# Kernel optimization log

Hardware: AMD Instinct MI355X
Metric: run time of the kernel (lower is better)

## Reference

```python
import jax, jax.numpy as jnp
import numpy as np

D_MODEL = 512
KERNEL = 16
DILATIONS = (1, 1, 2, 2, 4, 4, 8, 8)
HEADS = len(DILATIONS)
HEAD_W = D_MODEL // HEADS
B, L = 2, 1024
MODE = "forward"  # causal: window sees only prior words


def setup_inputs() -> dict:
    key = jax.random.key(0)
    ks = jax.random.split(key, 8)
    s = 0.02  # small init like nn.Linear
    return {
        "tensor": jax.random.normal(ks[0], (B, L, D_MODEL), jnp.float32),
        "Wq": jax.random.normal(ks[1], (HEADS, HEAD_W, D_MODEL), jnp.float32) * s,
        "bq": jnp.zeros((HEADS, HEAD_W), jnp.float32),
        "Wk": jax.random.normal(ks[2], (HEADS, KERNEL, HEAD_W, D_MODEL), jnp.float32) * s,
        "bk": jnp.zeros((HEADS, KERNEL, HEAD_W), jnp.float32),
        "Wv": jax.random.normal(ks[3], (HEADS, KERNEL, HEAD_W, D_MODEL), jnp.float32) * s,
        "bv": jnp.zeros((HEADS, KERNEL, HEAD_W), jnp.float32),
        "Wo": jax.random.normal(ks[4], (D_MODEL, HEADS, HEAD_W), jnp.float32) * s,
        "bo": jnp.zeros((D_MODEL,), jnp.float32),
    }


def _window_indices():
    """Static gather indices replicating Glimpses.dilocal's dilated unfold.

    Returns idx of shape (H, L, K) indexing into a sequence zero-padded by
    max_off on both sides: content[h, l, k] = x_padded[idx[h, l, k]].
    """
    dil = np.asarray(DILATIONS)  # (H,)
    max_off = int((KERNEL - 1) * dil.max())
    if MODE == "forward":
        front = (KERNEL - 1) * dil           # all padding in front (causal)
    elif MODE == "backward":
        front = np.zeros_like(dil)           # all padding behind
    else:  # center
        front = ((KERNEL - 1) * dil) // 2
    l = np.arange(L)[None, :, None]
    k = np.arange(KERNEL)[None, None, :]
    d = dil[:, None, None]
    f = front[:, None, None]
    idx = l + k * d - f + max_off            # (H, L, K), always in-range
    return jnp.asarray(idx), max_off


_IDX, _MOFF = _window_indices()


def reference(tensor, Wq, bq, Wk, bk, Wv, bv, Wo, bo):
    # tensor: (B, L, D)
    xp = jnp.pad(tensor, ((0, 0), (_MOFF, _MOFF), (0, 0)))
    content = xp[:, _IDX, :]                                   # (B,H,L,K,D)
    # per-head query projection (kernel position 1)
    q = jnp.einsum('bld,hod->bhlo', tensor, Wq) + bq[:, None, :]        # (B,H,L,hw)
    # per-(head, kernel-position) independent key/value projections
    k = jnp.einsum('bhlkd,hkod->bhlko', content, Wk) + bk[:, None, :, :]
    v = jnp.einsum('bhlkd,hkod->bhlko', content, Wv) + bv[:, None, :, :]
    # tiny local attention over the K window positions
    logits = jnp.einsum('bhlo,bhlko->bhlk', q, k)               # (B,H,L,K)
    score = jax.nn.softmax(logits, axis=-1)
    # NOTE: original scales AFTER the score@value matmul (faithful to source)
    attn = jnp.einsum('bhlk,bhlko->bhlo', score, v)
    attn = attn / jnp.sqrt(jnp.asarray(HEAD_W, tensor.dtype))   # (B,H,L,hw)
    # dehead: merge (heads, head_width) -> d_model
    out = jnp.einsum('bhlo,dho->bld', attn, Wo) + bo            # (B,L,D)
    return out
```

## Files before the change

### kernel.cpp

```cpp
#include <hip/hip_runtime.h>


#define BD 2
#define LL 1024
#define DM 512
#define HH 8
#define KT 16
#define HW 64

#define NQKV 16896

typedef unsigned short u16;
typedef unsigned int u32;
typedef __bf16 bf16x8 __attribute__((ext_vector_type(8)));
typedef float f32x4 __attribute__((ext_vector_type(4)));
typedef unsigned short ushort4v __attribute__((ext_vector_type(4)));
typedef unsigned short ushort8v __attribute__((ext_vector_type(8)));

__constant__ int c_dil[8] = {1, 1, 2, 2, 4, 4, 8, 8};

__device__ __forceinline__ float bf2f(u16 u) {
    return __builtin_bit_cast(float, (u32)u << 16);
}
__device__ __forceinline__ u16 f2bf(float f) {
    u32 u = __builtin_bit_cast(u32, f);
    return (u16)((u + 0x7fffu + ((u >> 16) & 1u)) >> 16);
}

__device__ __forceinline__ void gl_lds16(const u16* g, u16* l) {
    __builtin_amdgcn_global_load_lds(
        (__attribute__((address_space(1))) void*)g,
        (__attribute__((address_space(3))) void*)l, 16, 0, 0);
}

__global__ __launch_bounds__(256, 4) void gemm_bf16(
    const u16* __restrict__ A, const u16* __restrict__ Bm,
    const float* __restrict__ bq, const float* __restrict__ bk,
    const float* __restrict__ bv, u16* __restrict__ C)
{
    const int bid = blockIdx.x;
    const int wg  = (bid & 7) * 264 + (bid >> 3);
    const int m0  = (wg & 15) << 7;
    const int n0  = (wg >> 4) << 7;

    __shared__ u16 As[2][128 * 32];
    __shared__ u16 Bs[2][128 * 32];

    const int tid  = threadIdx.x;
    const int wave = tid >> 6, lane = tid & 63;
    const int r0 = tid >> 2;
    const int cc = (tid & 3) << 3;
    const int mw = (wave >> 1) << 6;
    const int nw = (wave & 1) << 6;
    const int lr = lane & 15;
    const int qg = lane >> 4;
    const int ksw = ((qg ^ ((lr >> 1) & 3)) << 3);

    const u16* Ag = A  + (size_t)(m0 + r0) * DM + cc;
    const u16* Bg = Bm + (size_t)(n0 + r0) * DM + cc;
    u16* lA = &As[0][0] + tid * 8;
    u16* lB = &Bs[0][0] + tid * 8;

#define STG(ko, c) do {                                                    \
        gl_lds16(Ag + (ko),                  lA + (c) * 4096);             \
        gl_lds16(Ag + (ko) + (size_t)64*DM,  lA + (c) * 4096 + 2048);      \
        gl_lds16(Bg + (ko),                  lB + (c) * 4096);             \
        gl_lds16(Bg + (ko) + (size_t)64*DM,  lB + (c) * 4096 + 2048);      \
    } while (0)

    f32x4 acc[4][4];
#pragma unroll
    for (int i = 0; i < 4; ++i)
#pragma unroll
        for (int j = 0; j < 4; ++j) acc[i][j] = (f32x4){0.f, 0.f, 0.f, 0.f};

    STG(0, 0);
    __syncthreads();

#pragma unroll
    for (int kc = 0; kc < 16; ++kc) {
        const int cur = kc & 1;
        if (kc < 15) STG((kc + 1) << 5, cur ^ 1);

        bf16x8 af[4], bfr[4];
#pragma unroll
        for (int i = 0; i < 4; ++i)
            af[i] = *(const bf16x8*)&As[cur][(mw + (i << 4) + lr) * 32 + ksw];
#pragma unroll
        for (int j = 0; j < 4; ++j)
            bfr[j] = *(const bf16x8*)&Bs[cur][(nw + (j << 4) + lr) * 32 + ksw];
#pragma unroll
        for (int i = 0; i < 4; ++i)
#pragma unroll
            for (int j = 0; j < 4; ++j)
                acc[i][j] = __builtin_amdgcn_mfma_f32_16x16x32_bf16(
                    af[i], bfr[j], acc[i][j], 0, 0, 0);

        __syncthreads();
    }
#undef STG

    const float* bias; int cb;
    if      (n0 <  512) { bias = bq; cb = 0;    }
    else if (n0 < 8704) { bias = bk; cb = 512;  }
    else                { bias = bv; cb = 8704; }

#pragma unroll
    for (int i = 0; i < 4; ++i) {
        const int rowb = m0 + mw + (i << 4) + (qg << 2);
#pragma unroll
        for (int j = 0; j < 4; ++j) {
            const int col = n0 + nw + (j << 4) + lr;
            const float bs = bias[col - cb];
#pragma unroll
            for (int r = 0; r < 4; ++r)
                C[(size_t)(rowb + r) * NQKV + col] = f2bf(acc[i][j][r] + bs);
        }
    }
}

__global__ __launch_bounds__(256, 4) void gemm_out(
    const u16* __restrict__ A, const u16* __restrict__ Bm,
    const float* __restrict__ bias, float* __restrict__ C)
{
    __shared__ u16 As[2][64 * 32];
    __shared__ u16 Bs[2][64 * 32];

    const int tid  = threadIdx.x;
    const int wave = tid >> 6, lane = tid & 63;
    const int m0 = blockIdx.y << 6, n0 = blockIdx.x << 6;
    const int r0 = tid >> 2, cc = (tid & 3) << 3;
    const int mw = wave << 4;
    const int lr = lane & 15, qg = lane >> 4;
    const int ksw = ((qg ^ ((lr >> 1) & 3)) << 3);

    const u16* Ag = A  + (size_t)(m0 + r0) * DM + cc;
    const u16* Bg = Bm + (size_t)(n0 + r0) * DM + cc;
    u16* lA = &As[0][0] + tid * 8;
    u16* lB = &Bs[0][0] + tid * 8;

#define STG(ko, c) do {                                                    \
        gl_lds16(Ag + (ko), lA + (c) * 2048);                              \
        gl_lds16(Bg + (ko), lB + (c) * 2048);                              \
    } while (0)

    f32x4 acc[4];
#pragma unroll
    for (int j = 0; j < 4; ++j) acc[j] = (f32x4){0.f, 0.f, 0.f, 0.f};

    STG(0, 0);
    __syncthreads();

#pragma unroll
    for (int kc = 0; kc < 16; ++kc) {
        const int cur = kc & 1;
        if (kc < 15) STG((kc + 1) << 5, cur ^ 1);

        bf16x8 af = *(const bf16x8*)&As[cur][(mw + lr) * 32 + ksw];
#pragma unroll
        for (int j = 0; j < 4; ++j) {
            bf16x8 bfr = *(const bf16x8*)&Bs[cur][((j << 4) + lr) * 32 + ksw];
            acc[j] = __builtin_amdgcn_mfma_f32_16x16x32_bf16(af, bfr, acc[j], 0, 0, 0);
        }
        __syncthreads();
    }
#undef STG

#pragma unroll
    for (int j = 0; j < 4; ++j) {
        const int col = n0 + (j << 4) + lr;
        const float bs = bias[col];
#pragma unroll
        for (int r = 0; r < 4; ++r)
            C[(size_t)(m0 + mw + (qg << 2) + r) * DM + col] = acc[j][r] + bs;
    }
}

__global__ void cvt_swz(const float* __restrict__ x,  const float* __restrict__ Wq,
                        const float* __restrict__ Wk, const float* __restrict__ Wv,
                        const float* __restrict__ Wo,
                        u16* __restrict__ xb, u16* __restrict__ wb,
                        u16* __restrict__ wob)
{
    const int i = blockIdx.x * 256 + threadIdx.x;
    const float* src; u16* dst; int t;
    if (i < 131072) {
        t = i;
        src = x;  dst = xb;
    } else if (i < 1212416) {
        t = i - 131072;
        const int row = t >> 6;
        if      (row <  512) src = Wq;
        else if (row < 8704) src = Wk - (size_t)512 * DM;
        else                 src = Wv - (size_t)8704 * DM;
        dst = wb;
    } else {
        t = i - 1212416;
        src = Wo; dst = wob;
    }
    const int row = t >> 6;
    const int c8  = t & 63;
    const int s   = (row >> 1) & 3;
    const int oc  = (c8 & ~3) | ((c8 & 3) ^ s);
    const float* p = src + (size_t)row * DM + (oc << 3);
    float4 v0 = *(const float4*)p;
    float4 v1 = *(const float4*)(p + 4);
    ushort8v o = { f2bf(v0.x), f2bf(v0.y), f2bf(v0.z), f2bf(v0.w),
                   f2bf(v1.x), f2bf(v1.y), f2bf(v1.z), f2bf(v1.w) };
    *(ushort8v*)(dst + (size_t)row * DM + (c8 << 3)) = o;
}

__global__ __launch_bounds__(256, 4) void attn_bf16(
    const u16* __restrict__ qkv,
    const float* __restrict__ bk,
    const float* __restrict__ bv,
    u16* __restrict__ attnb)
{
    const int tid = threadIdx.x;
    const int j  = tid & 7;
    const int ll = tid >> 3;
    const int bid = blockIdx.x;
    const int h = bid & 7;
    const int t = (bid >> 3) & 31;
    const int b = bid >> 8;
    const int l = (t << 5) + ll;
    const int dil = c_dil[h];

    const int hko = h * (KT * HW);
    const size_t rowbase = (size_t)(b * LL) * NQKV + hko + (j << 3);

    float qf[8];
    {
        ushort8v qv = *(const ushort8v*)(qkv + (size_t)(b * LL + l) * NQKV
                                         + h * HW + (j << 3));
#pragma unroll
        for (int z = 0; z < 8; ++z) qf[z] = bf2f(qv[z]);
    }

    ushort8v kr[KT];
#pragma unroll
    for (int k = 0; k < KT; ++k) {
        const int src = l - (KT - 1 - k) * dil;
        if (src >= 0)
            kr[k] = *(const ushort8v*)(qkv + rowbase + (size_t)src * NQKV
                                       + 512 + k * HW);
    }

    float lg[KT];
#pragma unroll
    for (int k = 0; k < KT; ++k) {
        const int src = l - (KT - 1 - k) * dil;
        float p = 0.f;
        if (src >= 0) {
#pragma unroll
            for (int z = 0; z < 8; ++z) p += qf[z] * bf2f(kr[k][z]);
        } else {
            const float* bkp = bk + hko + k * HW + (j << 3);
#pragma unroll
            for (int z = 0; z < 8; ++z) p += qf[z] * bkp[z];
        }
        p += __shfl_xor(p, 1);
        p += __shfl_xor(p, 2);
        p += __shfl_xor(p, 4);
        lg[k] = p;
    }

    float m = lg[0];
#pragma unroll
    for (int k = 1; k < KT; ++k) m = fmaxf(m, lg[k]);
    float s = 0.f;
#pragma unroll
    for (int k = 0; k < KT; ++k) { lg[k] = __expf(lg[k] - m); s += lg[k]; }
    const float inv = 1.f / s;

    ushort8v vr[KT];
#pragma unroll
    for (int k = 0; k < KT; ++k) {
        const int src = l - (KT - 1 - k) * dil;
        if (src >= 0)
            vr[k] = *(const ushort8v*)(qkv + rowbase + (size_t)src * NQKV
                                       + 8704 + k * HW);
    }

    float acc[8];
#pragma unroll
    for (int z = 0; z < 8; ++z) acc[z] = 0.f;
#pragma unroll
    for (int k = 0; k < KT; ++k) {
        const int src = l - (KT - 1 - k) * dil;
        const float sc = lg[k] * inv;
        if (src >= 0) {
#pragma unroll
            for (int z = 0; z < 8; ++z) acc[z] = fmaf(sc, bf2f(vr[k][z]), acc[z]);
        } else {
            const float* bvp = bv + hko + k * HW + (j << 3);
#pragma unroll
            for (int z = 0; z < 8; ++z) acc[z] = fmaf(sc, bvp[z], acc[z]);
        }
    }

    ushort8v o;
#pragma unroll
    for (int z = 0; z < 8; ++z) o[z] = f2bf(acc[z] * 0.125f);
    const int row = b * LL + l;
    const int k8 = h * 8 + j;
    const int sw = ((k8 & 3) ^ ((l >> 1) & 3)) << 3;
    *(ushort8v*)(attnb + (size_t)row * DM + ((k8 >> 2) << 5) + sw) = o;
}

__global__ __launch_bounds__(256, 2) void gemm_nt_bias(
    const float* __restrict__ A, const float* __restrict__ Bm,
    const float* __restrict__ bias, float* __restrict__ C,
    int M, int N, int Kd)
{
    __shared__ float As[16][68];
    __shared__ float Bs[16][68];
    const int tid = threadIdx.x;
    const int tx = tid & 15, ty = tid >> 4;
    const int r0 = blockIdx.y << 6, c0 = blockIdx.x << 6;
    const int lr = tid >> 2, k4 = (tid & 3) << 2;
    const float* Ap = A  + (size_t)(r0 + lr) * Kd + k4;
    const float* Bp = Bm + (size_t)(c0 + lr) * Kd + k4;
    float acc[4][4];
#pragma unroll
    for (int i = 0; i < 4; ++i)
#pragma unroll
        for (int j = 0; j < 4; ++j) acc[i][j] = 0.f;
    for (int d0 = 0; d0 < Kd; d0 += 16) {
        float4 av = *(const float4*)(Ap + d0);
        float4 bv = *(const float4*)(Bp + d0);
        As[k4 + 0][lr] = av.x; As[k4 + 1][lr] = av.y;
        As[k4 + 2][lr] = av.z; As[k4 + 3][lr] = av.w;
        Bs[k4 + 0][lr] = bv.x; Bs[k4 + 1][lr] = bv.y;
        Bs[k4 + 2][lr] = bv.z; Bs[k4 + 3][lr] = bv.w;
        __syncthreads();
#pragma unroll
        for (int dd = 0; dd < 16; ++dd) {
            float4 a4 = *(const float4*)&As[dd][ty << 2];
            float4 b4 = *(const float4*)&Bs[dd][tx << 2];
            float ar[4] = {a4.x, a4.y, a4.z, a4.w};
            float br[4] = {b4.x, b4.y, b4.z, b4.w};
#pragma unroll
            for (int i = 0; i < 4; ++i)
#pragma unroll
                for (int j = 0; j < 4; ++j)
                    acc[i][j] = fmaf(ar[i], br[j], acc[i][j]);
        }
        __syncthreads();
    }
#pragma unroll
    for (int i = 0; i < 4; ++i) {
        float4 o;
        const int c = c0 + (tx << 2);
        o.x = acc[i][0] + bias[c + 0];
        o.y = acc[i][1] + bias[c + 1];
        o.z = acc[i][2] + bias[c + 2];
        o.w = acc[i][3] + bias[c + 3];
        *(float4*)&C[(size_t)(r0 + (ty << 2) + i) * N + c] = o;
    }
}

__device__ __forceinline__ void tile_gemm_f32(
    const float* __restrict__ xb, int src, bool ok,
    const float* __restrict__ wrow,
    int lr, int k4, int tx, int ty,
    float (&As)[16][68], float (&Ws)[16][68], float (&acc)[4][4])
{
#pragma unroll
    for (int i = 0; i < 4; ++i)
#pragma unroll
        for (int j = 0; j < 4; ++j) acc[i][j] = 0.f;
    const float* xrow = xb + (size_t)(ok ? src : 0) * DM + k4;
    for (int d0 = 0; d0 < DM; d0 += 16) {
        float4 av = make_float4(0.f, 0.f, 0.f, 0.f);
        if (ok) av = *(const float4*)(xrow + d0);
        float4 wv = *(const float4*)(wrow + d0);
        As[k4 + 0][lr] = av.x; As[k4 + 1][lr] = av.y;
        As[k4 + 2][lr] = av.z; As[k4 + 3][lr] = av.w;
        Ws[k4 + 0][lr] = wv.x; Ws[k4 + 1][lr] = wv.y;
        Ws[k4 + 2][lr] = wv.z; Ws[k4 + 3][lr] = wv.w;
        __syncthreads();
#pragma unroll
        for (int dd = 0; dd < 16; ++dd) {
            float4 a4 = *(const float4*)&As[dd][ty << 2];
            float4 b4 = *(const float4*)&Ws[dd][tx << 2];
            float ar[4] = {a4.x, a4.y, a4.z, a4.w};
            float br[4] = {b4.x, b4.y, b4.z, b4.w};
#pragma unroll
            for (int i = 0; i < 4; ++i)
#pragma unroll
                for (int j = 0; j < 4; ++j)
                    acc[i][j] = fmaf(ar[i], br[j], acc[i][j]);
        }
        __syncthreads();
    }
}

__global__ __launch_bounds__(256, 2) void attn_kernel(
    const float* __restrict__ x, const float* __restrict__ q,
    const float* __restrict__ Wk, const float* __restrict__ bk,
    const float* __restrict__ Wv, const float* __restrict__ bv,
    float* __restrict__ attn)
{
    __shared__ float As[16][68];
    __shared__ float Ws[16][68];
    __shared__ float qs[64][68];
    __shared__ float lg[64][17];
    __shared__ float red[64][17];
    const int tid = threadIdx.x;
    const int tx = tid & 15, ty = tid >> 4;
    const int bid = blockIdx.x;
    const int h = bid & 7, t = (bid >> 3) & 15, b = bid >> 7;
    const int l0 = t << 6;
    const int dil = c_dil[h];
    const int lr = tid >> 2, k4 = (tid & 3) << 2;
    for (int i = tid; i < 64 * 16; i += 256) {
        int l = i >> 4, o4 = (i & 15) << 2;
        float4 v = *(const float4*)&q[((size_t)(b * LL + l0 + l) * HH + h) * HW + o4];
        *(float4*)&qs[l][o4] = v;
    }
    const float* xb  = x  + (size_t)b * LL * DM;
    const float* Wkh = Wk + (size_t)h * KT * HW * DM;
    const float* Wvh = Wv + (size_t)h * KT * HW * DM;
    const float* bkh = bk + h * KT * HW;
    const float* bvh = bv + h * KT * HW;
    float acc[4][4];
    for (int kk = 0; kk < KT; ++kk) {
        const int src = l0 + lr - (KT - 1 - kk) * dil;
        const bool ok = (src >= 0) && (src < LL);
        tile_gemm_f32(xb, src, ok, Wkh + (size_t)(kk * HW + lr) * DM + k4,
                      lr, k4, tx, ty, As, Ws, acc);
        const float* bkp = bkh + kk * HW + (tx << 2);
#pragma unroll
        for (int i = 0; i < 4; ++i) {
            float p = 0.f;
#pragma unroll
            for (int j = 0; j < 4; ++j)
                p += (acc[i][j] + bkp[j]) * qs[(ty << 2) + i][(tx << 2) + j];
            red[(ty << 2) + i][tx] = p;
        }
        __syncthreads();
        if (tid < 64) {
            float s = 0.f;
#pragma unroll
            for (int u = 0; u < 16; ++u) s += red[tid][u];
            lg[tid][kk] = s;
        }
        __syncthreads();
    }
    if (tid < 64) {
        float m = lg[tid][0];
#pragma unroll
        for (int u = 1; u < KT; ++u) m = fmaxf(m, lg[tid][u]);
        float s = 0.f;
#pragma unroll
        for (int u = 0; u < KT; ++u) {
            float e = expf(lg[tid][u] - m);
            lg[tid][u] = e; s += e;
        }
        float inv = 1.f / s;
#pragma unroll
        for (int u = 0; u < KT; ++u) lg[tid][u] *= inv;
    }
    __syncthreads();
    float vacc[4][4];
#pragma unroll
    for (int i = 0; i < 4; ++i)
#pragma unroll
        for (int j = 0; j < 4; ++j) vacc[i][j] = 0.f;
    for (int kk = 0; kk < KT; ++kk) {
        const int src = l0 + lr - (KT - 1 - kk) * dil;
        const bool ok = (src >= 0) && (src < LL);
        tile_gemm_f32(xb, src, ok, Wvh + (size_t)(kk * HW + lr) * DM + k4,
                      lr, k4, tx, ty, As, Ws, acc);
        const float* bvp = bvh + kk * HW + (tx << 2);
#pragma unroll
        for (int i = 0; i < 4; ++i) {
            float sc = lg[(ty << 2) + i][kk];
#pragma unroll
            for (int j = 0; j < 4; ++j)
                vacc[i][j] = fmaf(sc, acc[i][j] + bvp[j], vacc[i][j]);
        }
    }
#pragma unroll
    for (int i = 0; i < 4; ++i) {
        float4 o;
        o.x = vacc[i][0] * 0.125f;
        o.y = vacc[i][1] * 0.125f;
        o.z = vacc[i][2] * 0.125f;
        o.w = vacc[i][3] * 0.125f;
        *(float4*)&attn[((size_t)(b * LL + l0 + (ty << 2) + i) * HH + h) * HW + (tx << 2)] = o;
    }
}

extern "C" void kernel_launch(void* const* d_in, const int* in_sizes, int n_in,
                              void* d_out, int out_size, void* d_ws, size_t ws_size,
                              hipStream_t stream)
{
    const float* x  = (const float*)d_in[0];
    const float* Wq = (const float*)d_in[1];
    const float* bq = (const float*)d_in[2];
    const float* Wk = (const float*)d_in[3];
    const float* bk = (const float*)d_in[4];
    const float* Wv = (const float*)d_in[5];
    const float* bv = (const float*)d_in[6];
    const float* Wo = (const float*)d_in[7];
    const float* bo = (const float*)d_in[8];
    float* out = (float*)d_out;

    const int M = BD * LL;

    const size_t N_X   = (size_t)BD * LL * DM;
    const size_t N_WB  = (size_t)NQKV * DM;
    const size_t N_WO  = (size_t)DM * DM;
    const size_t N_QKV = (size_t)M * NQKV;
    const size_t NEED  = (N_X + N_WB + N_WO + N_QKV + N_X) * 2;

    if (ws_size >= NEED) {
        u16* xb    = (u16*)d_ws;
        u16* wb    = xb    + N_X;
        u16* wob   = wb    + N_WB;
        u16* qkv   = wob   + N_WO;
        u16* attnb = qkv   + N_QKV;

        cvt_swz<<<4864, 256, 0, stream>>>(x, Wq, Wk, Wv, Wo, xb, wb, wob);

        gemm_bf16<<<dim3(2112), 256, 0, stream>>>(
            xb, wb, bq, bk, bv, qkv);

        attn_bf16<<<BD * HH * (LL / 32), 256, 0, stream>>>(
            qkv, bk, bv, attnb);

        gemm_out<<<dim3(8, 32), 256, 0, stream>>>(attnb, wob, bo, out);
    } else {
        float* qws = (float*)d_ws;
        float* aws = qws + (size_t)BD * LL * HH * HW;
        gemm_nt_bias<<<dim3((HH * HW) / 64, M / 64), 256, 0, stream>>>(
            x, Wq, bq, qws, M, HH * HW, DM);
        attn_kernel<<<BD * HH * (LL / 64), 256, 0, stream>>>(
            x, qws, Wk, bk, Wv, bv, aws);
        gemm_nt_bias<<<dim3(DM / 64, M / 64), 256, 0, stream>>>(
            aws, Wo, bo, out, M, DM, HH * HW);
    }
}
```

Before: 171.5 us.

## Store K/V projections in per-slot contiguous layout for attention gathers

The QKV GEMM epilogue now writes Q into its own [M,512] buffer and scatters K and V into a [kv][head][kslot][batch][L][64] layout instead of one row-major [M,16896] matrix. In the attention kernel, each window gather then reads 64-element contiguous rows inside a compact per-(head,slot) plane, rather than striding by 16896 elements per row. This should improve cache and TLB locality for the dilated gathers. In exchange, the GEMM stores are scattered across planes with per-row index arithmetic, which may coalesce less well.

```diff
diff --git a/kernel.cpp b/kernel.cpp
--- a/kernel.cpp
+++ b/kernel.cpp
@@ -36,7 +36,8 @@
 __global__ __launch_bounds__(256, 4) void gemm_bf16(
     const u16* __restrict__ A, const u16* __restrict__ Bm,
     const float* __restrict__ bq, const float* __restrict__ bk,
-    const float* __restrict__ bv, u16* __restrict__ C)
+    const float* __restrict__ bv,
+    u16* __restrict__ qb, u16* __restrict__ kvb)
 {
     const int bid = blockIdx.x;
     const int wg  = (bid & 7) * 264 + (bid >> 3);
@@ -100,21 +101,43 @@
     }
 #undef STG
 
-    const float* bias; int cb;
-    if      (n0 <  512) { bias = bq; cb = 0;    }
-    else if (n0 < 8704) { bias = bk; cb = 512;  }
-    else                { bias = bv; cb = 8704; }
-
-#pragma unroll
-    for (int i = 0; i < 4; ++i) {
-        const int rowb = m0 + mw + (i << 4) + (qg << 2);
-#pragma unroll
-        for (int j = 0; j < 4; ++j) {
-            const int col = n0 + nw + (j << 4) + lr;
-            const float bs = bias[col - cb];
-#pragma unroll
-            for (int r = 0; r < 4; ++r)
-                C[(size_t)(rowb + r) * NQKV + col] = f2bf(acc[i][j][r] + bs);
+    if (n0 < 512) {
+#pragma unroll
+        for (int i = 0; i < 4; ++i) {
+            const int rowb = m0 + mw + (i << 4) + (qg << 2);
+#pragma unroll
+            for (int j = 0; j < 4; ++j) {
+                const int col = n0 + nw + (j << 4) + lr;
+                const float bs = bq[col];
+#pragma unroll
+                for (int r = 0; r < 4; ++r)
+                    qb[(size_t)(rowb + r) * 512 + col] =
+                        f2bf(acc[i][j][r] + bs);
+            }
+        }
+    } else {
+        const int reg = (n0 >= 8704);
+        const float* bias = reg ? bv : bk;
+        const int t0  = n0 - (reg ? 8704 : 512);
+        const int h   = t0 >> 10;
+        const int pb  = ((reg << 3) + h) << 4;
+#pragma unroll
+        for (int i = 0; i < 4; ++i) {
+            const int rowb = m0 + mw + (i << 4) + (qg << 2);
+#pragma unroll
+            for (int j = 0; j < 4; ++j) {
+                const int tcol  = (t0 & 1023) + nw + (j << 4) + lr;
+                const int kslot = tcol >> 6;
+                const int oo    = tcol & 63;
+                const float bs  = bias[(h << 10) + tcol];
+#pragma unroll
+                for (int r = 0; r < 4; ++r) {
+                    const int row = rowb + r;
+                    const int bb  = row >> 10, l2 = row & 1023;
+                    kvb[((size_t)(((pb + kslot) << 1) + bb) << 16)
+                        + (l2 << 6) + oo] = f2bf(acc[i][j][r] + bs);
+                }
+            }
         }
     }
 }
@@ -211,7 +234,8 @@
 }
 
 __global__ __launch_bounds__(256, 4) void attn_bf16(
-    const u16* __restrict__ qkv,
+    const u16* __restrict__ qb,
+    const u16* __restrict__ kvb,
     const float* __restrict__ bk,
     const float* __restrict__ bv,
     u16* __restrict__ attnb)
@@ -227,23 +251,24 @@
     const int dil = c_dil[h];
 
     const int hko = h * (KT * HW);
-    const size_t rowbase = (size_t)(b * LL) * NQKV + hko + (j << 3);
 
     float qf[8];
     {
-        ushort8v qv = *(const ushort8v*)(qkv + (size_t)(b * LL + l) * NQKV
+        ushort8v qv = *(const ushort8v*)(qb + (size_t)(b * LL + l) * 512
                                          + h * HW + (j << 3));
 #pragma unroll
         for (int z = 0; z < 8; ++z) qf[z] = bf2f(qv[z]);
     }
+
+    const u16* kbase = kvb + ((size_t)(((h << 4) << 1) + b) << 16) + (j << 3);
+    const u16* vbase = kbase + ((size_t)(8 << 4) << 17);
 
     ushort8v kr[KT];
 #pragma unroll
     for (int k = 0; k < KT; ++k) {
         const int src = l - (KT - 1 - k) * dil;
         if (src >= 0)
-            kr[k] = *(const ushort8v*)(qkv + rowbase + (size_t)src * NQKV
-                                       + 512 + k * HW);
+            kr[k] = *(const ushort8v*)(kbase + ((size_t)k << 17) + (src << 6));
     }
 
     float lg[KT];
@@ -278,8 +303,7 @@
     for (int k = 0; k < KT; ++k) {
         const int src = l - (KT - 1 - k) * dil;
         if (src >= 0)
-            vr[k] = *(const ushort8v*)(qkv + rowbase + (size_t)src * NQKV
-                                       + 8704 + k * HW);
+            vr[k] = *(const ushort8v*)(vbase + ((size_t)k << 17) + (src << 6));
     }
 
     float acc[8];
@@ -520,16 +544,17 @@
         u16* xb    = (u16*)d_ws;
         u16* wb    = xb    + N_X;
         u16* wob   = wb    + N_WB;
-        u16* qkv   = wob   + N_WO;
-        u16* attnb = qkv   + N_QKV;
+        u16* qb    = wob   + N_WO;
+        u16* kvb   = qb    + N_X;
+        u16* attnb = qb    + N_QKV;
 
         cvt_swz<<<4864, 256, 0, stream>>>(x, Wq, Wk, Wv, Wo, xb, wb, wob);
 
         gemm_bf16<<<dim3(2112), 256, 0, stream>>>(
-            xb, wb, bq, bk, bv, qkv);
+            xb, wb, bq, bk, bv, qb, kvb);
 
         attn_bf16<<<BD * HH * (LL / 32), 256, 0, stream>>>(
-            qkv, bk, bv, attnb);
+            qb, kvb, bk, bv, attnb);
 
         gemm_out<<<dim3(8, 32), 256, 0, stream>>>(attnb, wob, bo, out);
     } else {
```

After: 171.9 us. About the same (+0.2%).
